# Optimization experiments

Hardware: AMD Instinct MI355X
Metric: run time of the kernel (lower is better)

## Reference

```python
import jax, jax.numpy as jnp
import numpy as np

EMB = 4096
NUM_EXPERTS = 64
TOP_K = 2
TOKENS = 16384


def setup_inputs() -> dict:
    key = jax.random.key(0)
    kx, kw, kb = jax.random.split(key, 3)
    x = jax.random.normal(kx, (TOKENS, EMB), dtype=jnp.float32)
    # nn.Linear(emb_size, num_experts): weight [num_experts, emb], bias [num_experts]
    W = jax.random.normal(kw, (NUM_EXPERTS, EMB), dtype=jnp.float32) / np.sqrt(EMB)
    b = jax.random.normal(kb, (NUM_EXPERTS,), dtype=jnp.float32) * 0.01
    return {"x": x, "W": W, "b": b}


def reference(x, W, b):
    # logits = x @ W.T + b  -> [tokens, num_experts]
    logits = jnp.einsum("td,ed->te", x, W) + b
    topk_val, topk_idx = jax.lax.top_k(logits, TOP_K)  # [tokens, k]
    probs = jax.nn.softmax(topk_val, axis=-1)
    return (topk_idx, probs)
```

## Files before the change

### kernel.cpp

```cpp
#include <hip/hip_runtime.h>

#define TOKENS 16384
#define EMB 4096
#define NEXP 64
#define BK 32
#define KSP 4
#define KPER (EMB / KSP)
#define NCH (KPER / BK)
#define NMM (NCH / 2)

typedef __attribute__((ext_vector_type(8))) short short8;
typedef __attribute__((ext_vector_type(4))) float f32x4;
typedef __attribute__((ext_vector_type(4))) unsigned short ush4;

#define WP_USHORTS (3 * NEXP * EMB)
#define WP_FLOATS  (WP_USHORTS / 2)

__device__ __forceinline__ void gl_lds16(const void* g, void* lds) {
    __builtin_amdgcn_global_load_lds(
        (const __attribute__((address_space(1))) void*)g,
        (__attribute__((address_space(3))) void*)lds, 16, 0, 0);
}

__device__ __forceinline__ void split3(float x, unsigned short& h,
                                       unsigned short& m, unsigned short& l) {
    unsigned u = __float_as_uint(x);
    unsigned r = u + 0x7FFFu + ((u >> 16) & 1u);
    float hF = __uint_as_float(r & 0xFFFF0000u);
    h = (unsigned short)(r >> 16);
    float r1 = x - hF;
    unsigned u1 = __float_as_uint(r1);
    float mF = __uint_as_float(u1 & 0xFFFF0000u);
    m = (unsigned short)(u1 >> 16);
    float r2 = r1 - mF;
    l = (unsigned short)(__float_as_uint(r2) >> 16);
}

__device__ __forceinline__ void split3_pair(float x0, float x1,
        unsigned& hw, unsigned& mw, unsigned& lw) {
    unsigned u0 = __float_as_uint(x0), u1 = __float_as_uint(x1);
    unsigned r0 = u0 + 0x7FFFu + ((u0 >> 16) & 1u);
    unsigned r1 = u1 + 0x7FFFu + ((u1 >> 16) & 1u);
    hw = __builtin_amdgcn_perm(r1, r0, 0x07060302u);
    float s0 = x0 - __uint_as_float(r0 & 0xFFFF0000u);
    float s1 = x1 - __uint_as_float(r1 & 0xFFFF0000u);
    unsigned v0 = __float_as_uint(s0), v1 = __float_as_uint(s1);
    mw = __builtin_amdgcn_perm(v1, v0, 0x07060302u);
    float t0 = s0 - __uint_as_float(v0 & 0xFFFF0000u);
    float t1 = s1 - __uint_as_float(v1 & 0xFFFF0000u);
    lw = __builtin_amdgcn_perm(__float_as_uint(t1), __float_as_uint(t0), 0x07060302u);
}

__device__ __forceinline__ void build_frags(const float4& a0, const float4& a1,
        short8& H, short8& M, short8& L) {
    union { short8 v; unsigned u[4]; } h_, m_, l_;
    split3_pair(a0.x, a0.y, h_.u[0], m_.u[0], l_.u[0]);
    split3_pair(a0.z, a0.w, h_.u[1], m_.u[1], l_.u[1]);
    split3_pair(a1.x, a1.y, h_.u[2], m_.u[2], l_.u[2]);
    split3_pair(a1.z, a1.w, h_.u[3], m_.u[3], l_.u[3]);
    H = h_.v; M = m_.v; L = l_.v;
}

__global__ __launch_bounds__(256) void split_w(const float* __restrict__ W,
                                               unsigned short* __restrict__ Wp) {
    const int i = (blockIdx.x * 256 + threadIdx.x) * 4;
    const float4 v = *reinterpret_cast<const float4*>(W + i);
    ush4 h, m, l;
#pragma unroll
    for (int e = 0; e < 4; ++e) {
        unsigned short he, me, le;
        split3(reinterpret_cast<const float*>(&v)[e], he, me, le);
        h[e] = he; m[e] = me; l[e] = le;
    }
    *reinterpret_cast<ush4*>(Wp + i) = h;
    *reinterpret_cast<ush4*>(Wp + NEXP * EMB + i) = m;
    *reinterpret_cast<ush4*>(Wp + 2 * NEXP * EMB + i) = l;
}

#define MFMA_BLOCK(BUFC, AH0, AM0, AL0, AH1, AM1, AL1)                          \
    _Pragma("unroll")                                                           \
    for (int et = 0; et < 4; ++et) {                                            \
        const unsigned short* bp = &sB[g][BUFC][et * 16 + lr][lo * 8];          \
        const short8 bH = *reinterpret_cast<const short8*>(bp);                 \
        const short8 bM = *reinterpret_cast<const short8*>(bp + 64 * BK);       \
        const short8 bL = *reinterpret_cast<const short8*>(bp + 128 * BK);      \
        accH[0][et] = __builtin_amdgcn_mfma_f32_16x16x32_bf16(AH0, bH, accH[0][et], 0, 0, 0); \
        accL[0][et] = __builtin_amdgcn_mfma_f32_16x16x32_bf16(AH0, bM, accL[0][et], 0, 0, 0); \
        accL[0][et] = __builtin_amdgcn_mfma_f32_16x16x32_bf16(AM0, bH, accL[0][et], 0, 0, 0); \
        accL[0][et] = __builtin_amdgcn_mfma_f32_16x16x32_bf16(AM0, bM, accL[0][et], 0, 0, 0); \
        accL[0][et] = __builtin_amdgcn_mfma_f32_16x16x32_bf16(AH0, bL, accL[0][et], 0, 0, 0); \
        accL[0][et] = __builtin_amdgcn_mfma_f32_16x16x32_bf16(AL0, bH, accL[0][et], 0, 0, 0); \
        accH[1][et] = __builtin_amdgcn_mfma_f32_16x16x32_bf16(AH1, bH, accH[1][et], 0, 0, 0); \
        accL[1][et] = __builtin_amdgcn_mfma_f32_16x16x32_bf16(AH1, bM, accL[1][et], 0, 0, 0); \
        accL[1][et] = __builtin_amdgcn_mfma_f32_16x16x32_bf16(AM1, bH, accL[1][et], 0, 0, 0); \
        accL[1][et] = __builtin_amdgcn_mfma_f32_16x16x32_bf16(AM1, bM, accL[1][et], 0, 0, 0); \
        accL[1][et] = __builtin_amdgcn_mfma_f32_16x16x32_bf16(AH1, bL, accL[1][et], 0, 0, 0); \
        accL[1][et] = __builtin_amdgcn_mfma_f32_16x16x32_bf16(AL1, bH, accL[1][et], 0, 0, 0); \
    }

#define ISSUE_B(CHUNK, BUF)                                                     \
    _Pragma("unroll")                                                           \
    for (int p = 0; p < 6; ++p)                                                 \
        gl_lds16(gb[p] + (CHUNK) * BK, &sB[g][BUF][16 * (6 * h + p)][0]);

#define ISSUE_A(MACRO, ASET)                                                    \
    _Pragma("unroll")                                                           \
    for (int ti = 0; ti < 2; ++ti) {                                            \
        const float* ab_ = ax[ti] + 2 * (MACRO) * BK;                           \
        ASET[ti][0][0] = *reinterpret_cast<const float4*>(ab_);                 \
        ASET[ti][0][1] = *reinterpret_cast<const float4*>(ab_ + 4);             \
        ASET[ti][1][0] = *reinterpret_cast<const float4*>(ab_ + BK);            \
        ASET[ti][1][1] = *reinterpret_cast<const float4*>(ab_ + BK + 4);        \
    }

#define COMPUTE(ASET, CI, BUFC) do {                                            \
    short8 aH0, aM0, aL0, aH1, aM1, aL1;                                        \
    build_frags(ASET[0][CI][0], ASET[0][CI][1], aH0, aM0, aL0);                 \
    build_frags(ASET[1][CI][0], ASET[1][CI][1], aH1, aM1, aL1);                 \
    MFMA_BLOCK(BUFC, aH0, aM0, aL0, aH1, aM1, aL1)                              \
} while (0)

#define BODY(MM, ACUR, ANXT, BC0, BC1, BC2, ISLAST) do {                        \
    ISSUE_B(2 * (MM) + 1, BC1);                                         \
    if (!(ISLAST)) { ISSUE_A((MM) + 1, ANXT); }                         \
    __builtin_amdgcn_sched_barrier(0);                                          \
    if (ISLAST) asm volatile("s_waitcnt vmcnt(6)" ::: "memory");        \
    else        asm volatile("s_waitcnt vmcnt(14)" ::: "memory");               \
    __builtin_amdgcn_s_barrier();                                       \
    __builtin_amdgcn_sched_barrier(0);                                          \
    COMPUTE(ACUR, 0, BC0);                                              \
    if (!(ISLAST)) { ISSUE_B(2 * (MM) + 2, BC2); }                      \
    __builtin_amdgcn_sched_barrier(0);                                          \
    if (ISLAST) asm volatile("s_waitcnt vmcnt(0)" ::: "memory");        \
    else        asm volatile("s_waitcnt vmcnt(14)" ::: "memory");               \
    __builtin_amdgcn_s_barrier();                                       \
    __builtin_amdgcn_sched_barrier(0);                                          \
    COMPUTE(ACUR, 1, BC1);                                              \
} while (0)

__global__ __launch_bounds__(512) void router_fused(
    const float* __restrict__ x, const unsigned short* __restrict__ Wp,
    const float* __restrict__ b, float* __restrict__ out)
{
    __shared__ unsigned short sB[KSP][3][192][BK];

    const int t  = threadIdx.x;
    const int w  = t >> 6;
    const int l  = t & 63;
    const int g  = w >> 1;
    const int h  = w & 1;
    const int lr = l & 15;
    const int lo = l >> 4;
    const int tokB = blockIdx.x * 64;
    const int tok0 = tokB + h * 32;
    const int kb   = g * KPER;

    const float* ax[2];
    ax[0] = x + (size_t)(tok0 + lr) * EMB + kb + lo * 8;
    ax[1] = ax[0] + (size_t)16 * EMB;

    const unsigned short* gb[6];
#pragma unroll
    for (int p = 0; p < 6; ++p)
        gb[p] = Wp + (size_t)(16 * (6 * h + p) + (l >> 2)) * EMB + kb + 8 * (l & 3);

    f32x4 accH[2][4], accL[2][4];
#pragma unroll
    for (int ti = 0; ti < 2; ++ti)
#pragma unroll
        for (int et = 0; et < 4; ++et) {
            accH[ti][et] = (f32x4){0.f, 0.f, 0.f, 0.f};
            accL[ti][et] = (f32x4){0.f, 0.f, 0.f, 0.f};
        }

    float4 aA[2][2][2], aB[2][2][2];
    ISSUE_A(0, aA);
    __builtin_amdgcn_sched_barrier(0);
    ISSUE_B(0, 0);
    __builtin_amdgcn_sched_barrier(0);

#pragma unroll 1
    for (int mb = 0; mb < 12; mb += 6) {
        BODY(mb + 0, aA, aB, 0, 1, 2, false);
        BODY(mb + 1, aB, aA, 2, 0, 1, false);
        BODY(mb + 2, aA, aB, 1, 2, 0, false);
        BODY(mb + 3, aB, aA, 0, 1, 2, false);
        BODY(mb + 4, aA, aB, 2, 0, 1, false);
        BODY(mb + 5, aB, aA, 1, 2, 0, false);
    }
    BODY(12, aA, aB, 0, 1, 2, false);
    BODY(13, aB, aA, 2, 0, 1, false);
    BODY(14, aA, aB, 1, 2, 0, false);
    BODY(15, aB, aA, 0, 1, 2, true);

    __syncthreads();
    float* logits = reinterpret_cast<float*>(&sB[0][0][0][0]);
#pragma unroll
    for (int ti = 0; ti < 2; ++ti)
#pragma unroll
        for (int et = 0; et < 4; ++et)
#pragma unroll
            for (int j = 0; j < 4; ++j) {
                const int ltok = h * 32 + ti * 16 + lo * 4 + j;
                logits[(g * 64 + ltok) * 65 + et * 16 + lr]
                    = accH[ti][et][j] + accL[ti][et][j];
            }
    __syncthreads();

    double* sv = reinterpret_cast<double*>(logits + KSP * 64 * 65);
    int*    si = reinterpret_cast<int*>(sv + 64 * 8 * 2);

    const int tok  = t >> 3;
    const int part = t & 7;
    double v[8];
#pragma unroll
    for (int j = 0; j < 8; ++j) v[j] = 0.0;
#pragma unroll
    for (int gg = 0; gg < KSP; ++gg)
#pragma unroll
        for (int j = 0; j < 8; ++j)
            v[j] += (double)logits[(gg * 64 + tok) * 65 + part * 8 + j];
#pragma unroll
    for (int j = 0; j < 8; ++j) v[j] += (double)b[part * 8 + j];

    double v1 = -1e300, v2 = -1e300; int i1 = 0, i2 = 0;
#pragma unroll
    for (int j = 0; j < 8; ++j) {
        const int e = part * 8 + j;
        if (v[j] > v1)      { v2 = v1; i2 = i1; v1 = v[j]; i1 = e; }
        else if (v[j] > v2) { v2 = v[j]; i2 = e; }
    }
    sv[(tok * 8 + part) * 2 + 0] = v1;
    sv[(tok * 8 + part) * 2 + 1] = v2;
    si[(tok * 8 + part) * 2 + 0] = i1;
    si[(tok * 8 + part) * 2 + 1] = i2;
    __syncthreads();

    if (part == 0) {
        double m1 = -1e300, m2 = -1e300; int j1 = 0, j2 = 0;
#pragma unroll
        for (int p = 0; p < 8; ++p)
#pragma unroll
            for (int r = 0; r < 2; ++r) {
                const double vv = sv[(tok * 8 + p) * 2 + r];
                const int    ii = si[(tok * 8 + p) * 2 + r];
                if (vv > m1)      { m2 = m1; j2 = j1; m1 = vv; j1 = ii; }
                else if (vv > m2) { m2 = vv; j2 = ii; }
            }
        const float e2  = expf((float)(m2 - m1));
        const float inv = 1.0f / (1.0f + e2);
        const int gt = tokB + tok;
        out[2 * gt]     = (float)j1;
        out[2 * gt + 1] = (float)j2;
        out[2 * TOKENS + 2 * gt]     = inv;
        out[2 * TOKENS + 2 * gt + 1] = e2 * inv;
    }
}

extern "C" void kernel_launch(void* const* d_in, const int* in_sizes, int n_in,
                              void* d_out, int out_size, void* d_ws, size_t ws_size,
                              hipStream_t stream) {
    const float* x = (const float*)d_in[0];
    const float* W = (const float*)d_in[1];
    const float* b = (const float*)d_in[2];
    float* out = (float*)d_out;
    unsigned short* Wp = (unsigned short*)d_ws;

    split_w<<<dim3(NEXP * EMB / 1024), dim3(256), 0, stream>>>(W, Wp);
    router_fused<<<dim3(TOKENS / 64), dim3(512), 0, stream>>>(x, Wp, b, out);
}
```

Baseline: 85.65 us.

## Give each wave a private LDS pipeline and halve the K-split to remove block barriers

The main loop is reorganised so each of the 8 waves owns a 32-token by 32-expert tile. Each wave double-buffers its own W slice in private LDS and synchronises only with s_waitcnt, with no block-wide s_barrier. The K-split drops from 4 to 2, so each wave covers a longer K range, and x fragments are prefetched two chunks ahead. The cost is duplicated traffic: W chunks are loaded separately by the two token-halves, and each x row is loaded by the two expert-halves. That roughly doubles global and L2 requests for the dominant x stream.

```diff
diff --git a/kernel.cpp b/kernel.cpp
--- a/kernel.cpp
+++ b/kernel.cpp
@@ -4,10 +4,9 @@
 #define EMB 4096
 #define NEXP 64
 #define BK 32
-#define KSP 4
+#define KSP 2
 #define KPER (EMB / KSP)
 #define NCH (KPER / BK)
-#define NMM (NCH / 2)
 
 typedef __attribute__((ext_vector_type(8))) short short8;
 typedef __attribute__((ext_vector_type(4))) float f32x4;
@@ -77,13 +76,25 @@
     *reinterpret_cast<ush4*>(Wp + 2 * NEXP * EMB + i) = l;
 }
 
+#define ISSUE_B(C, BUF)                                                         \
+    _Pragma("unroll")                                                           \
+    for (int q = 0; q < 6; ++q)                                                 \
+        gl_lds16(gbw[q] + (C) * BK, &sBw[BUF][16 * q][0]);
+
+#define ISSUE_A(C, ASET)                                                        \
+    _Pragma("unroll")                                                           \
+    for (int ti = 0; ti < 2; ++ti) {                                            \
+        ASET[ti][0] = *reinterpret_cast<const float4*>(ax[ti] + (C) * BK);      \
+        ASET[ti][1] = *reinterpret_cast<const float4*>(ax[ti] + (C) * BK + 4);  \
+    }
+
 #define MFMA_BLOCK(BUFC, AH0, AM0, AL0, AH1, AM1, AL1)                          \
     _Pragma("unroll")                                                           \
-    for (int et = 0; et < 4; ++et) {                                            \
-        const unsigned short* bp = &sB[g][BUFC][et * 16 + lr][lo * 8];          \
+    for (int et = 0; et < 2; ++et) {                                            \
+        const unsigned short* bp = &sBw[BUFC][et * 16 + lr][lo * 8];            \
         const short8 bH = *reinterpret_cast<const short8*>(bp);                 \
-        const short8 bM = *reinterpret_cast<const short8*>(bp + 64 * BK);       \
-        const short8 bL = *reinterpret_cast<const short8*>(bp + 128 * BK);      \
+        const short8 bM = *reinterpret_cast<const short8*>(bp + 32 * BK);       \
+        const short8 bL = *reinterpret_cast<const short8*>(bp + 64 * BK);       \
         accH[0][et] = __builtin_amdgcn_mfma_f32_16x16x32_bf16(AH0, bH, accH[0][et], 0, 0, 0); \
         accL[0][et] = __builtin_amdgcn_mfma_f32_16x16x32_bf16(AH0, bM, accL[0][et], 0, 0, 0); \
         accL[0][et] = __builtin_amdgcn_mfma_f32_16x16x32_bf16(AM0, bH, accL[0][et], 0, 0, 0); \
@@ -98,111 +109,85 @@
         accL[1][et] = __builtin_amdgcn_mfma_f32_16x16x32_bf16(AL1, bH, accL[1][et], 0, 0, 0); \
     }
 
-#define ISSUE_B(CHUNK, BUF)                                                     \
-    _Pragma("unroll")                                                           \
-    for (int p = 0; p < 6; ++p)                                                 \
-        gl_lds16(gb[p] + (CHUNK) * BK, &sB[g][BUF][16 * (6 * h + p)][0]);
-
-#define ISSUE_A(MACRO, ASET)                                                    \
-    _Pragma("unroll")                                                           \
-    for (int ti = 0; ti < 2; ++ti) {                                            \
-        const float* ab_ = ax[ti] + 2 * (MACRO) * BK;                           \
-        ASET[ti][0][0] = *reinterpret_cast<const float4*>(ab_);                 \
-        ASET[ti][0][1] = *reinterpret_cast<const float4*>(ab_ + 4);             \
-        ASET[ti][1][0] = *reinterpret_cast<const float4*>(ab_ + BK);            \
-        ASET[ti][1][1] = *reinterpret_cast<const float4*>(ab_ + BK + 4);        \
-    }
-
-#define COMPUTE(ASET, CI, BUFC) do {                                            \
+#define ITER(C, ASET, BUFC, VM, DO_B, DO_A) do {                                \
+    asm volatile("s_waitcnt vmcnt(" #VM ")" ::: "memory");                      \
+    __builtin_amdgcn_sched_barrier(0);                                          \
+    if (DO_B) { ISSUE_B((C) + 1, (BUFC) ^ 1); }                                 \
+    __builtin_amdgcn_sched_barrier(0);        \
     short8 aH0, aM0, aL0, aH1, aM1, aL1;                                        \
-    build_frags(ASET[0][CI][0], ASET[0][CI][1], aH0, aM0, aL0);                 \
-    build_frags(ASET[1][CI][0], ASET[1][CI][1], aH1, aM1, aL1);                 \
+    build_frags(ASET[0][0], ASET[0][1], aH0, aM0, aL0);                         \
+    build_frags(ASET[1][0], ASET[1][1], aH1, aM1, aL1);                         \
+    if (DO_A) { ISSUE_A((C) + 2, ASET); }                                       \
+    __builtin_amdgcn_sched_barrier(0);    \
     MFMA_BLOCK(BUFC, aH0, aM0, aL0, aH1, aM1, aL1)                              \
-} while (0)
-
-#define BODY(MM, ACUR, ANXT, BC0, BC1, BC2, ISLAST) do {                        \
-    ISSUE_B(2 * (MM) + 1, BC1);                                         \
-    if (!(ISLAST)) { ISSUE_A((MM) + 1, ANXT); }                         \
-    __builtin_amdgcn_sched_barrier(0);                                          \
-    if (ISLAST) asm volatile("s_waitcnt vmcnt(6)" ::: "memory");        \
-    else        asm volatile("s_waitcnt vmcnt(14)" ::: "memory");               \
-    __builtin_amdgcn_s_barrier();                                       \
-    __builtin_amdgcn_sched_barrier(0);                                          \
-    COMPUTE(ACUR, 0, BC0);                                              \
-    if (!(ISLAST)) { ISSUE_B(2 * (MM) + 2, BC2); }                      \
-    __builtin_amdgcn_sched_barrier(0);                                          \
-    if (ISLAST) asm volatile("s_waitcnt vmcnt(0)" ::: "memory");        \
-    else        asm volatile("s_waitcnt vmcnt(14)" ::: "memory");               \
-    __builtin_amdgcn_s_barrier();                                       \
-    __builtin_amdgcn_sched_barrier(0);                                          \
-    COMPUTE(ACUR, 1, BC1);                                              \
 } while (0)
 
 __global__ __launch_bounds__(512) void router_fused(
     const float* __restrict__ x, const unsigned short* __restrict__ Wp,
     const float* __restrict__ b, float* __restrict__ out)
 {
-    __shared__ unsigned short sB[KSP][3][192][BK];
+    __shared__ unsigned short sB[8][2][96][BK];
 
     const int t  = threadIdx.x;
     const int w  = t >> 6;
     const int l  = t & 63;
-    const int g  = w >> 1;
     const int h  = w & 1;
+    const int e2 = (w >> 1) & 1;
+    const int g  = w >> 2;
     const int lr = l & 15;
     const int lo = l >> 4;
     const int tokB = blockIdx.x * 64;
     const int tok0 = tokB + h * 32;
+    const int eb   = e2 * 32;
     const int kb   = g * KPER;
+
+    unsigned short (*sBw)[96][BK] = sB[w];
 
     const float* ax[2];
     ax[0] = x + (size_t)(tok0 + lr) * EMB + kb + lo * 8;
     ax[1] = ax[0] + (size_t)16 * EMB;
 
-    const unsigned short* gb[6];
-#pragma unroll
-    for (int p = 0; p < 6; ++p)
-        gb[p] = Wp + (size_t)(16 * (6 * h + p) + (l >> 2)) * EMB + kb + 8 * (l & 3);
-
-    f32x4 accH[2][4], accL[2][4];
+    const unsigned short* gbw[6];
+#pragma unroll
+    for (int q = 0; q < 6; ++q)
+        gbw[q] = Wp + (size_t)((q >> 1) * 64 + eb + (q & 1) * 16 + (l >> 2)) * EMB
+               + kb + 8 * (l & 3);
+
+    f32x4 accH[2][2], accL[2][2];
 #pragma unroll
     for (int ti = 0; ti < 2; ++ti)
 #pragma unroll
-        for (int et = 0; et < 4; ++et) {
+        for (int et = 0; et < 2; ++et) {
             accH[ti][et] = (f32x4){0.f, 0.f, 0.f, 0.f};
             accL[ti][et] = (f32x4){0.f, 0.f, 0.f, 0.f};
         }
 
-    float4 aA[2][2][2], aB[2][2][2];
+    float4 aA[2][2], aB[2][2];
+    ISSUE_B(0, 0);
+    __builtin_amdgcn_sched_barrier(0);
     ISSUE_A(0, aA);
     __builtin_amdgcn_sched_barrier(0);
-    ISSUE_B(0, 0);
+    ISSUE_A(1, aB);
     __builtin_amdgcn_sched_barrier(0);
 
 #pragma unroll 1
-    for (int mb = 0; mb < 12; mb += 6) {
-        BODY(mb + 0, aA, aB, 0, 1, 2, false);
-        BODY(mb + 1, aB, aA, 2, 0, 1, false);
-        BODY(mb + 2, aA, aB, 1, 2, 0, false);
-        BODY(mb + 3, aB, aA, 0, 1, 2, false);
-        BODY(mb + 4, aA, aB, 2, 0, 1, false);
-        BODY(mb + 5, aB, aA, 1, 2, 0, false);
-    }
-    BODY(12, aA, aB, 0, 1, 2, false);
-    BODY(13, aB, aA, 2, 0, 1, false);
-    BODY(14, aA, aB, 1, 2, 0, false);
-    BODY(15, aB, aA, 0, 1, 2, true);
+    for (int cc = 0; cc < NCH - 2; cc += 2) {
+        ITER(cc,     aA, 0, 4, true, true);
+        ITER(cc + 1, aB, 1, 4, true, true);
+    }
+    ITER(NCH - 2, aA, 0, 4, true,  false);
+    ITER(NCH - 1, aB, 1, 0, false, false);
 
     __syncthreads();
     float* logits = reinterpret_cast<float*>(&sB[0][0][0][0]);
 #pragma unroll
     for (int ti = 0; ti < 2; ++ti)
 #pragma unroll
-        for (int et = 0; et < 4; ++et)
+        for (int et = 0; et < 2; ++et)
 #pragma unroll
             for (int j = 0; j < 4; ++j) {
                 const int ltok = h * 32 + ti * 16 + lo * 4 + j;
-                logits[(g * 64 + ltok) * 65 + et * 16 + lr]
+                logits[(g * 64 + ltok) * 65 + eb + et * 16 + lr]
                     = accH[ti][et][j] + accL[ti][et][j];
             }
     __syncthreads();
@@ -247,13 +232,13 @@
                 if (vv > m1)      { m2 = m1; j2 = j1; m1 = vv; j1 = ii; }
                 else if (vv > m2) { m2 = vv; j2 = ii; }
             }
-        const float e2  = expf((float)(m2 - m1));
-        const float inv = 1.0f / (1.0f + e2);
+        const float e2s = expf((float)(m2 - m1));
+        const float inv = 1.0f / (1.0f + e2s);
         const int gt = tokB + tok;
         out[2 * gt]     = (float)j1;
         out[2 * gt + 1] = (float)j2;
         out[2 * TOKENS + 2 * gt]     = inv;
-        out[2 * TOKENS + 2 * gt + 1] = e2 * inv;
+        out[2 * TOKENS + 2 * gt + 1] = e2s * inv;
     }
 }
 
```

After: 121.7 us. +42.0%, slower.
